# Performance work log

Measured on AMD Instinct MI355X. Metric: run time of the kernel, lower is better.

## Reference

```python
import jax, jax.numpy as jnp
import numpy as np

ALPHA = jnp.full((8,), 0.25, dtype=jnp.float32)  # per-class focal alpha
GAMMA = 2.0
TEMP = 0.07
CIRC_TARGET = 1.0
CIRC_WEIGHT = 0.1
MIN_AGREE = 0.6
W_FOCAL, W_CONTRAST, W_CONSENSUS = 1.0, 0.5, 0.3


def setup_inputs() -> dict:
    key = jax.random.key(0)
    k1, k2, k3, k4, k5 = jax.random.split(key, 5)
    return {
        "logits": jax.random.normal(k1, (32, 8, 256, 256), dtype=jnp.float32),
        "target": jax.random.randint(k2, (32, 256, 256), 0, 8, dtype=jnp.int32),
        "features": jax.random.normal(k3, (1024, 512), dtype=jnp.float32),
        "masks": jax.random.uniform(k4, (32, 3, 256, 256), dtype=jnp.float32),
        "method_preds": jax.random.uniform(k5, (3, 32, 256, 256), dtype=jnp.float32),
    }


def focal_loss(logits, target):
    B, C, H, W = logits.shape
    x = logits.transpose(0, 2, 3, 1).reshape(-1, C)  # [BHW, C]
    t = target.reshape(-1)
    logp = jax.nn.log_softmax(x, axis=-1)
    ce = -jnp.take_along_axis(logp, t[:, None], axis=1)[:, 0]
    p = jnp.exp(-ce)
    focal_w = ALPHA[t] * (1.0 - p) ** GAMMA
    return jnp.mean(focal_w * ce)


def contrastive_loss(features):
    Bf = features.shape[0]
    f = features / jnp.linalg.norm(features, axis=1, keepdims=True)
    sim = (f @ f.T) / TEMP  # [Bf, Bf]
    # default labels = arange(Bf//2) tiled twice -> each sample has exactly one
    # positive: its paired view at index (i + Bf//2) % Bf
    pos_idx = (jnp.arange(Bf) + Bf // 2) % Bf
    pos = sim[jnp.arange(Bf), pos_idx]
    diag = jnp.eye(Bf, dtype=bool)
    # logits row i = {positive_i} U negatives_i = all j != i (single positive case)
    masked = jnp.where(diag, -1e30, sim)
    lse = jax.nn.logsumexp(masked, axis=1)
    return jnp.mean(lse - pos)  # CE with target = the (only) positive


def circularity_loss(masks):
    m = masks[:, 0]  # [B, H, W] core channel
    B = m.shape[0]
    area = jnp.sum(m, axis=(1, 2))
    ex = jnp.sum(jnp.abs(m[:, 1:, :] - m[:, :-1, :]), axis=(1, 2))
    ey = jnp.sum(jnp.abs(m[:, :, 1:] - m[:, :, :-1]), axis=(1, 2))
    per = ex + ey
    circ = 4.0 * np.pi * area / jnp.maximum(per, 1e-12) ** 2
    li = jnp.where((area > 0) & (per > 0), (circ - CIRC_TARGET) ** 2, 0.0)
    return CIRC_WEIGHT * jnp.sum(li) / B


def consensus_loss(method_preds):
    K = method_preds.shape[0]
    total, n = 0.0, 0
    for i in range(K):  # K=3 methods -> 3 pairs (fixed, small)
        for j in range(i + 1, K):
            pi, pj = method_preds[i], method_preds[j]
            inter = jnp.sum(pi * pj)
            union = jnp.sum(pi + pj - pi * pj)
            iou = inter / (union + 1e-6)
            total = total + jax.nn.relu(MIN_AGREE - iou)
            n += 1
    return total / n


def reference(logits, target, features, masks, method_preds):
    return (W_FOCAL * focal_loss(logits, target)
            + W_CONTRAST * contrastive_loss(features)
            + circularity_loss(masks)
            + W_CONSENSUS * consensus_loss(method_preds))
```

## Files before the change

kernel.cpp:

```cpp
#include <hip/hip_runtime.h>
#include <math.h>

#define WS_FOCALP 0
#define WS_CONSP  2048
#define WS_AREAP  14336
#define WS_EXP_   14848
#define WS_EYP_   15360
#define WS_POS    15872
#define WS_PART   16896
#define WS_HI_B   393216
#define WS_LO_B   1441792

typedef __attribute__((ext_vector_type(8))) short bf16x8;
typedef __attribute__((ext_vector_type(4))) float f32x4;

__device__ inline float wave_reduce(float v) {
#pragma unroll
  for (int m = 32; m >= 1; m >>= 1) v += __shfl_xor(v, m);
  return v;
}

__device__ inline unsigned short bf16_rne(float x) {
  union { float f; unsigned u; } v; v.f = x;
  unsigned r = v.u + 0x7FFF + ((v.u >> 16) & 1);
  return (unsigned short)(r >> 16);
}
__device__ inline float bf16_f(unsigned short h) {
  union { unsigned u; float f; } v; v.u = ((unsigned)h) << 16; return v.f;
}

__device__ inline float focal_px(float v0, float v1, float v2, float v3,
                                 float v4, float v5, float v6, float v7, int tt) {
  float mx = fmaxf(fmaxf(fmaxf(v0, v1), fmaxf(v2, v3)),
                   fmaxf(fmaxf(v4, v5), fmaxf(v6, v7)));
  float se = __expf(v0 - mx) + __expf(v1 - mx) + __expf(v2 - mx) + __expf(v3 - mx) +
             __expf(v4 - mx) + __expf(v5 - mx) + __expf(v6 - mx) + __expf(v7 - mx);
  float xt = v0;
  xt = (tt == 1) ? v1 : xt;
  xt = (tt == 2) ? v2 : xt;
  xt = (tt == 3) ? v3 : xt;
  xt = (tt == 4) ? v4 : xt;
  xt = (tt == 5) ? v5 : xt;
  xt = (tt == 6) ? v6 : xt;
  xt = (tt == 7) ? v7 : xt;
  float lp = (xt - mx) - __logf(se);
  float p = __expf(lp);
  float om = 1.0f - p;
  return 0.25f * om * om * (-lp);
}

__global__ __launch_bounds__(256) void prep_kernel(const float* __restrict__ feat,
                                                   float* __restrict__ ws) {
  const int tid = threadIdx.x;
  const int lane = tid & 63;
  const int wid = tid >> 6;
  int row = blockIdx.x * 4 + wid;
  const float4* f4 = (const float4*)feat;
  float4 u = f4[row * 128 + lane];
  float4 w = f4[row * 128 + 64 + lane];
  float s = u.x * u.x + u.y * u.y + u.z * u.z + u.w * u.w +
            w.x * w.x + w.y * w.y + w.z * w.z + w.w * w.w;
  s = wave_reduce(s);
  float scale = 3.7796447300922719f / sqrtf(s);
  float g[8] = {u.x * scale, u.y * scale, u.z * scale, u.w * scale,
                w.x * scale, w.y * scale, w.z * scale, w.w * scale};
  unsigned short h[8];
  unsigned short l[8];
#pragma unroll
  for (int i = 0; i < 8; i++) {
    h[i] = bf16_rne(g[i]);
    l[i] = bf16_rne(g[i] - bf16_f(h[i]));
  }
  char* hb = (char*)ws + WS_HI_B + row * 1024;
  char* lb = (char*)ws + WS_LO_B + row * 1024;
  *(ushort4*)(hb + lane * 8) = make_ushort4(h[0], h[1], h[2], h[3]);
  *(ushort4*)(hb + 512 + lane * 8) = make_ushort4(h[4], h[5], h[6], h[7]);
  *(ushort4*)(lb + lane * 8) = make_ushort4(l[0], l[1], l[2], l[3]);
  *(ushort4*)(lb + 512 + lane * 8) = make_ushort4(l[4], l[5], l[6], l[7]);
}

__global__ __launch_bounds__(256) void fused_kernel(
    const float* __restrict__ logits, const int* __restrict__ target,
    const float* __restrict__ masks, const float* __restrict__ preds,
    float* __restrict__ ws) {
  __shared__ float red[32];
  const int bid = blockIdx.x;
  const int tid = threadIdx.x;
  const int lane = tid & 63;
  const int wid = tid >> 6;

  if (bid < 128) {
    const int rt = bid >> 3, ct = bid & 7;
    const int wr = wid >> 1, wc = wid & 1;
    const int l15 = lane & 15;
    const int hi8 = lane >> 4;
    const char* HI = (const char*)ws + WS_HI_B;
    const char* LO = (const char*)ws + WS_LO_B;
    const int ar = rt * 64 + wr * 32 + l15;
    const int bc = ct * 128 + wc * 64 + l15;
    const int kb16 = hi8 * 16;

    f32x4 acc[2][4];
#pragma unroll
    for (int r = 0; r < 2; r++)
#pragma unroll
      for (int c = 0; c < 4; c++) acc[r][c] = (f32x4){0.f, 0.f, 0.f, 0.f};

#pragma unroll 2
    for (int kb = 0; kb < 16; kb++) {
      int ko = kb * 64 + kb16;
      bf16x8 ah[2], al[2], bh[4], bl[4];
#pragma unroll
      for (int r = 0; r < 2; r++) {
        ah[r] = *(const bf16x8*)(HI + (ar + r * 16) * 1024 + ko);
        al[r] = *(const bf16x8*)(LO + (ar + r * 16) * 1024 + ko);
      }
#pragma unroll
      for (int c = 0; c < 4; c++) {
        bh[c] = *(const bf16x8*)(HI + (bc + c * 16) * 1024 + ko);
        bl[c] = *(const bf16x8*)(LO + (bc + c * 16) * 1024 + ko);
      }
#pragma unroll
      for (int r = 0; r < 2; r++)
#pragma unroll
        for (int c = 0; c < 4; c++) {
          acc[r][c] = __builtin_amdgcn_mfma_f32_16x16x32_bf16(ah[r], bh[c], acc[r][c], 0, 0, 0);
          acc[r][c] = __builtin_amdgcn_mfma_f32_16x16x32_bf16(ah[r], bl[c], acc[r][c], 0, 0, 0);
          acc[r][c] = __builtin_amdgcn_mfma_f32_16x16x32_bf16(al[r], bh[c], acc[r][c], 0, 0, 0);
        }
    }

    float2* part = (float2*)(ws + WS_PART);
#pragma unroll
    for (int r = 0; r < 2; r++)
#pragma unroll
      for (int q = 0; q < 4; q++) {
        int row = rt * 64 + wr * 32 + r * 16 + hi8 * 4 + q;
        int pc = (row + 512) & 1023;
        float m = -3e38f;
        float v[4];
#pragma unroll
        for (int c = 0; c < 4; c++) {
          int col = ct * 128 + wc * 64 + c * 16 + l15;
          float x = acc[r][c][q];
          if (col == pc) ws[WS_POS + row] = x;
          if (col == row) x = -1e30f;
          v[c] = x;
          m = fmaxf(m, x);
        }
        float s = 0.f;
#pragma unroll
        for (int c = 0; c < 4; c++) s += __expf(v[c] - m);
#pragma unroll
        for (int d = 1; d < 16; d <<= 1) {
          float mo = __shfl_xor(m, d), so = __shfl_xor(s, d);
          float nm = fmaxf(m, mo);
          s = s * __expf(m - nm) + so * __expf(mo - nm);
          m = nm;
        }
        if (l15 == 0) part[row * 16 + ct * 2 + wc] = make_float2(m, s);
      }
    return;
  }

  const int bid2 = bid - 128;

  if (bid2 < 2048) {
    int t = bid2 * 256 + tid;
    int p4 = t * 4;
    int b = p4 >> 16;
    int hw = p4 & 65535;
    const float* lb = logits + (b << 19) + hw;
    float4 x0 = *(const float4*)(lb + (0 << 16));
    float4 x1 = *(const float4*)(lb + (1 << 16));
    float4 x2 = *(const float4*)(lb + (2 << 16));
    float4 x3 = *(const float4*)(lb + (3 << 16));
    float4 x4 = *(const float4*)(lb + (4 << 16));
    float4 x5 = *(const float4*)(lb + (5 << 16));
    float4 x6 = *(const float4*)(lb + (6 << 16));
    float4 x7 = *(const float4*)(lb + (7 << 16));
    int4 tg = *(const int4*)(target + p4);
    float acc = 0.0f;
    acc += focal_px(x0.x, x1.x, x2.x, x3.x, x4.x, x5.x, x6.x, x7.x, tg.x);
    acc += focal_px(x0.y, x1.y, x2.y, x3.y, x4.y, x5.y, x6.y, x7.y, tg.y);
    acc += focal_px(x0.z, x1.z, x2.z, x3.z, x4.z, x5.z, x6.z, x7.z, tg.z);
    acc += focal_px(x0.w, x1.w, x2.w, x3.w, x4.w, x5.w, x6.w, x7.w, tg.w);
    float v = wave_reduce(acc);
    if (lane == 0) red[wid] = v;
    __syncthreads();
    if (tid == 0) ws[WS_FOCALP + bid2] = red[0] + red[1] + red[2] + red[3];

  } else if (bid2 < 2560) {
    int bi = bid2 - 2048;
    int img = bi >> 4;
    int part = bi & 15;
    const float* mS = masks + img * 3 * 65536;
    const float4* m4 = (const float4*)mS;
    float a = 0.0f, ex = 0.0f, ey = 0.0f;
#pragma unroll
    for (int i = 0; i < 4; i++) {
      int v = tid + 256 * i;
      int rl = v >> 6;
      int c4 = v & 63;
      int row = part * 16 + rl;
      float4 val = m4[row * 64 + c4];
      a += val.x + val.y + val.z + val.w;
      ey += fabsf(val.y - val.x) + fabsf(val.z - val.y) + fabsf(val.w - val.z);
      if (c4 > 0) ey += fabsf(val.x - mS[row * 256 + c4 * 4 - 1]);
      if (row > 0) {
        float4 u = m4[(row - 1) * 64 + c4];
        ex += fabsf(val.x - u.x) + fabsf(val.y - u.y) +
              fabsf(val.z - u.z) + fabsf(val.w - u.w);
      }
    }
    float ra = wave_reduce(a);
    float rx = wave_reduce(ex);
    float ry = wave_reduce(ey);
    if (lane == 0) {
      red[wid + 0] = ra; red[wid + 4] = rx; red[wid + 8] = ry;
    }
    __syncthreads();
    if (tid == 0) {
      ws[WS_AREAP + bi] = red[0] + red[1] + red[2] + red[3];
      ws[WS_EXP_ + bi] = red[4] + red[5] + red[6] + red[7];
      ws[WS_EYP_ + bi] = red[8] + red[9] + red[10] + red[11];
    }

  } else {
    int b = bid2 - 2560;
    int t = b * 256 + tid;
    const float4* q = (const float4*)preds;
    float4 a0 = q[t];
    float4 a1 = q[t + 524288];
    float4 a2 = q[t + 1048576];
    float s0 = a0.x + a0.y + a0.z + a0.w;
    float s1 = a1.x + a1.y + a1.z + a1.w;
    float s2 = a2.x + a2.y + a2.z + a2.w;
    float p01 = a0.x * a1.x + a0.y * a1.y + a0.z * a1.z + a0.w * a1.w;
    float p02 = a0.x * a2.x + a0.y * a2.y + a0.z * a2.z + a0.w * a2.w;
    float p12 = a1.x * a2.x + a1.y * a2.y + a1.z * a2.z + a1.w * a2.w;
    float r0 = wave_reduce(s0);
    float r1 = wave_reduce(s1);
    float r2 = wave_reduce(s2);
    float r3 = wave_reduce(p01);
    float r4 = wave_reduce(p02);
    float r5 = wave_reduce(p12);
    if (lane == 0) {
      red[wid + 0] = r0; red[wid + 4] = r1; red[wid + 8] = r2;
      red[wid + 12] = r3; red[wid + 16] = r4; red[wid + 20] = r5;
    }
    __syncthreads();
    if (tid == 0) {
#pragma unroll
      for (int k = 0; k < 6; k++)
        ws[WS_CONSP + k * 2048 + b] =
            red[k * 4] + red[k * 4 + 1] + red[k * 4 + 2] + red[k * 4 + 3];
    }
  }
}

__device__ inline float block_reduce_1024(float v, float* red) {
  int tid = threadIdx.x;
  v = wave_reduce(v);
  __syncthreads();
  if ((tid & 63) == 0) red[tid >> 6] = v;
  __syncthreads();
  float t = 0.0f;
  if (tid == 0) {
#pragma unroll
    for (int i = 0; i < 16; i++) t += red[i];
  }
  return t;
}

__global__ __launch_bounds__(1024) void final_kernel(float* __restrict__ ws,
                                                     float* __restrict__ out) {
  __shared__ float red[16];
  __shared__ float li_s[32];
  int r = threadIdx.x;

  const float2* part = (const float2*)(ws + WS_PART);
  float M = -1e30f, S = 0.0f;
#pragma unroll
  for (int ctl = 0; ctl < 16; ctl++) {
    float2 p = part[r * 16 + ctl];
    float nm = fmaxf(M, p.x);
    S = S * __expf(M - nm) + p.y * __expf(p.x - nm);
    M = nm;
  }
  float lse = M + __logf(S);
  float contr_sum = block_reduce_1024(lse - ws[WS_POS + r], red);

  float focal_sum =
      block_reduce_1024(ws[WS_FOCALP + r] + ws[WS_FOCALP + r + 1024], red);

  float cons[6];
#pragma unroll
  for (int k = 0; k < 6; k++) {
    const float* p = ws + WS_CONSP + k * 2048;
    cons[k] = block_reduce_1024(p[r] + p[r + 1024], red);
  }

  float li = 0.0f;
  if (r < 512) {
    float a = ws[WS_AREAP + r];
    float ex = ws[WS_EXP_ + r];
    float ey = ws[WS_EYP_ + r];
#pragma unroll
    for (int d = 1; d < 16; d <<= 1) {
      a += __shfl_xor(a, d);
      ex += __shfl_xor(ex, d);
      ey += __shfl_xor(ey, d);
    }
    if ((r & 15) == 0) {
      float per = ex + ey;
      float dd = fmaxf(per, 1e-12f);
      float c = 12.566370614359172f * a / (dd * dd);
      li = (a > 0.0f && per > 0.0f) ? (c - 1.0f) * (c - 1.0f) : 0.0f;
      li_s[r >> 4] = li;
    }
  }
  __syncthreads();

  if (r == 0) {
    float circ = 0.0f;
#pragma unroll
    for (int i = 0; i < 32; i++) circ += li_s[i];
    circ = 0.1f * circ / 32.0f;

    float contr = contr_sum / 1024.0f;
    float focal = focal_sum / 2097152.0f;

    float S0 = cons[0], S1 = cons[1], S2 = cons[2];
    float P01 = cons[3], P02 = cons[4], P12 = cons[5];
    float co = 0.0f;
    co += fmaxf(0.6f - P01 / (S0 + S1 - P01 + 1e-6f), 0.0f);
    co += fmaxf(0.6f - P02 / (S0 + S2 - P02 + 1e-6f), 0.0f);
    co += fmaxf(0.6f - P12 / (S1 + S2 - P12 + 1e-6f), 0.0f);
    co *= (1.0f / 3.0f);

    out[0] = focal + 0.5f * contr + circ + 0.3f * co;
  }
}

extern "C" void kernel_launch(void* const* d_in, const int* in_sizes, int n_in,
                              void* d_out, int out_size, void* d_ws, size_t ws_size,
                              hipStream_t stream) {
  const float* logits = (const float*)d_in[0];
  const int* target = (const int*)d_in[1];
  const float* feat = (const float*)d_in[2];
  const float* masks = (const float*)d_in[3];
  const float* preds = (const float*)d_in[4];
  float* ws = (float*)d_ws;
  float* out = (float*)d_out;

  prep_kernel<<<256, 256, 0, stream>>>(feat, ws);
  fused_kernel<<<4736, 256, 0, stream>>>(logits, target, masks, preds, ws);
  final_kernel<<<1, 1024, 0, stream>>>(ws, out);
}
```

Measured before the change: 54.36 us.

## Move feature prep into streaming kernel and split similarity GEMM into own kernel

Feature normalisation and bf16 hi/lo splitting now run as extra blocks at the end of the main streaming kernel, which removes the separate prep launch. The similarity GEMM moves to its own kernel afterwards, using smaller 64x64 tiles over 256 blocks so more CUs share the work, which doubles the partial logsumexp entries per row. The final kernel replaces eight sequential block reductions with one batched wave-reduce pass and a single barrier. In exchange, the GEMM no longer overlaps with the bandwidth-bound streaming work and now runs serially after it.

```diff
diff --git a/kernel.cpp b/kernel.cpp
--- a/kernel.cpp
+++ b/kernel.cpp
@@ -49,124 +49,18 @@
   return 0.25f * om * om * (-lp);
 }
 
-__global__ __launch_bounds__(256) void prep_kernel(const float* __restrict__ feat,
-                                                   float* __restrict__ ws) {
-  const int tid = threadIdx.x;
-  const int lane = tid & 63;
-  const int wid = tid >> 6;
-  int row = blockIdx.x * 4 + wid;
-  const float4* f4 = (const float4*)feat;
-  float4 u = f4[row * 128 + lane];
-  float4 w = f4[row * 128 + 64 + lane];
-  float s = u.x * u.x + u.y * u.y + u.z * u.z + u.w * u.w +
-            w.x * w.x + w.y * w.y + w.z * w.z + w.w * w.w;
-  s = wave_reduce(s);
-  float scale = 3.7796447300922719f / sqrtf(s);
-  float g[8] = {u.x * scale, u.y * scale, u.z * scale, u.w * scale,
-                w.x * scale, w.y * scale, w.z * scale, w.w * scale};
-  unsigned short h[8];
-  unsigned short l[8];
-#pragma unroll
-  for (int i = 0; i < 8; i++) {
-    h[i] = bf16_rne(g[i]);
-    l[i] = bf16_rne(g[i] - bf16_f(h[i]));
-  }
-  char* hb = (char*)ws + WS_HI_B + row * 1024;
-  char* lb = (char*)ws + WS_LO_B + row * 1024;
-  *(ushort4*)(hb + lane * 8) = make_ushort4(h[0], h[1], h[2], h[3]);
-  *(ushort4*)(hb + 512 + lane * 8) = make_ushort4(h[4], h[5], h[6], h[7]);
-  *(ushort4*)(lb + lane * 8) = make_ushort4(l[0], l[1], l[2], l[3]);
-  *(ushort4*)(lb + 512 + lane * 8) = make_ushort4(l[4], l[5], l[6], l[7]);
-}
-
-__global__ __launch_bounds__(256) void fused_kernel(
+__global__ __launch_bounds__(256) void mega_kernel(
     const float* __restrict__ logits, const int* __restrict__ target,
-    const float* __restrict__ masks, const float* __restrict__ preds,
-    float* __restrict__ ws) {
+    const float* __restrict__ feat, const float* __restrict__ masks,
+    const float* __restrict__ preds, float* __restrict__ ws) {
   __shared__ float red[32];
   const int bid = blockIdx.x;
   const int tid = threadIdx.x;
   const int lane = tid & 63;
   const int wid = tid >> 6;
 
-  if (bid < 128) {
-    const int rt = bid >> 3, ct = bid & 7;
-    const int wr = wid >> 1, wc = wid & 1;
-    const int l15 = lane & 15;
-    const int hi8 = lane >> 4;
-    const char* HI = (const char*)ws + WS_HI_B;
-    const char* LO = (const char*)ws + WS_LO_B;
-    const int ar = rt * 64 + wr * 32 + l15;
-    const int bc = ct * 128 + wc * 64 + l15;
-    const int kb16 = hi8 * 16;
-
-    f32x4 acc[2][4];
-#pragma unroll
-    for (int r = 0; r < 2; r++)
-#pragma unroll
-      for (int c = 0; c < 4; c++) acc[r][c] = (f32x4){0.f, 0.f, 0.f, 0.f};
-
-#pragma unroll 2
-    for (int kb = 0; kb < 16; kb++) {
-      int ko = kb * 64 + kb16;
-      bf16x8 ah[2], al[2], bh[4], bl[4];
-#pragma unroll
-      for (int r = 0; r < 2; r++) {
-        ah[r] = *(const bf16x8*)(HI + (ar + r * 16) * 1024 + ko);
-        al[r] = *(const bf16x8*)(LO + (ar + r * 16) * 1024 + ko);
-      }
-#pragma unroll
-      for (int c = 0; c < 4; c++) {
-        bh[c] = *(const bf16x8*)(HI + (bc + c * 16) * 1024 + ko);
-        bl[c] = *(const bf16x8*)(LO + (bc + c * 16) * 1024 + ko);
-      }
-#pragma unroll
-      for (int r = 0; r < 2; r++)
-#pragma unroll
-        for (int c = 0; c < 4; c++) {
-          acc[r][c] = __builtin_amdgcn_mfma_f32_16x16x32_bf16(ah[r], bh[c], acc[r][c], 0, 0, 0);
-          acc[r][c] = __builtin_amdgcn_mfma_f32_16x16x32_bf16(ah[r], bl[c], acc[r][c], 0, 0, 0);
-          acc[r][c] = __builtin_amdgcn_mfma_f32_16x16x32_bf16(al[r], bh[c], acc[r][c], 0, 0, 0);
-        }
-    }
-
-    float2* part = (float2*)(ws + WS_PART);
-#pragma unroll
-    for (int r = 0; r < 2; r++)
-#pragma unroll
-      for (int q = 0; q < 4; q++) {
-        int row = rt * 64 + wr * 32 + r * 16 + hi8 * 4 + q;
-        int pc = (row + 512) & 1023;
-        float m = -3e38f;
-        float v[4];
-#pragma unroll
-        for (int c = 0; c < 4; c++) {
-          int col = ct * 128 + wc * 64 + c * 16 + l15;
-          float x = acc[r][c][q];
-          if (col == pc) ws[WS_POS + row] = x;
-          if (col == row) x = -1e30f;
-          v[c] = x;
-          m = fmaxf(m, x);
-        }
-        float s = 0.f;
-#pragma unroll
-        for (int c = 0; c < 4; c++) s += __expf(v[c] - m);
-#pragma unroll
-        for (int d = 1; d < 16; d <<= 1) {
-          float mo = __shfl_xor(m, d), so = __shfl_xor(s, d);
-          float nm = fmaxf(m, mo);
-          s = s * __expf(m - nm) + so * __expf(mo - nm);
-          m = nm;
-        }
-        if (l15 == 0) part[row * 16 + ct * 2 + wc] = make_float2(m, s);
-      }
-    return;
-  }
-
-  const int bid2 = bid - 128;
-
-  if (bid2 < 2048) {
-    int t = bid2 * 256 + tid;
+  if (bid < 2048) {
+    int t = bid * 256 + tid;
     int p4 = t * 4;
     int b = p4 >> 16;
     int hw = p4 & 65535;
@@ -188,10 +82,10 @@
     float v = wave_reduce(acc);
     if (lane == 0) red[wid] = v;
     __syncthreads();
-    if (tid == 0) ws[WS_FOCALP + bid2] = red[0] + red[1] + red[2] + red[3];
-
-  } else if (bid2 < 2560) {
-    int bi = bid2 - 2048;
+    if (tid == 0) ws[WS_FOCALP + bid] = red[0] + red[1] + red[2] + red[3];
+
+  } else if (bid < 2560) {
+    int bi = bid - 2048;
     int img = bi >> 4;
     int part = bi & 15;
     const float* mS = masks + img * 3 * 65536;
@@ -226,8 +120,8 @@
       ws[WS_EYP_ + bi] = red[8] + red[9] + red[10] + red[11];
     }
 
-  } else {
-    int b = bid2 - 2560;
+  } else if (bid < 4608) {
+    int b = bid - 2560;
     int t = b * 256 + tid;
     const float4* q = (const float4*)preds;
     float4 a0 = q[t];
@@ -256,52 +150,138 @@
         ws[WS_CONSP + k * 2048 + b] =
             red[k * 4] + red[k * 4 + 1] + red[k * 4 + 2] + red[k * 4 + 3];
     }
-  }
-}
-
-__device__ inline float block_reduce_1024(float v, float* red) {
-  int tid = threadIdx.x;
-  v = wave_reduce(v);
-  __syncthreads();
-  if ((tid & 63) == 0) red[tid >> 6] = v;
-  __syncthreads();
-  float t = 0.0f;
-  if (tid == 0) {
-#pragma unroll
-    for (int i = 0; i < 16; i++) t += red[i];
-  }
-  return t;
+
+  } else {
+    int row = (bid - 4608) * 4 + wid;
+    const float4* f4 = (const float4*)feat;
+    float4 u = f4[row * 128 + lane];
+    float4 w = f4[row * 128 + 64 + lane];
+    float s = u.x * u.x + u.y * u.y + u.z * u.z + u.w * u.w +
+              w.x * w.x + w.y * w.y + w.z * w.z + w.w * w.w;
+    s = wave_reduce(s);
+    float scale = 3.7796447300922719f / sqrtf(s);
+    float g[8] = {u.x * scale, u.y * scale, u.z * scale, u.w * scale,
+                  w.x * scale, w.y * scale, w.z * scale, w.w * scale};
+    unsigned short h[8];
+    unsigned short l[8];
+#pragma unroll
+    for (int i = 0; i < 8; i++) {
+      h[i] = bf16_rne(g[i]);
+      l[i] = bf16_rne(g[i] - bf16_f(h[i]));
+    }
+    char* hb = (char*)ws + WS_HI_B + row * 1024;
+    char* lb = (char*)ws + WS_LO_B + row * 1024;
+    *(ushort4*)(hb + lane * 8) = make_ushort4(h[0], h[1], h[2], h[3]);
+    *(ushort4*)(hb + 512 + lane * 8) = make_ushort4(h[4], h[5], h[6], h[7]);
+    *(ushort4*)(lb + lane * 8) = make_ushort4(l[0], l[1], l[2], l[3]);
+    *(ushort4*)(lb + 512 + lane * 8) = make_ushort4(l[4], l[5], l[6], l[7]);
+  }
+}
+
+__global__ __launch_bounds__(256) void sim_kernel(float* __restrict__ ws) {
+  const int tid = threadIdx.x;
+  const int lane = tid & 63;
+  const int wid = tid >> 6;
+  const int rt = blockIdx.x >> 4, ct = blockIdx.x & 15;
+  const int wr = wid >> 1, wc = wid & 1;
+  const int l15 = lane & 15;
+  const int hi8 = lane >> 4;
+  const char* HI = (const char*)ws + WS_HI_B;
+  const char* LO = (const char*)ws + WS_LO_B;
+  const int ar = rt * 64 + wr * 32 + l15;
+  const int bc = ct * 64 + wc * 32 + l15;
+  const int kb16 = hi8 * 16;
+
+  f32x4 acc[2][2];
+#pragma unroll
+  for (int r = 0; r < 2; r++)
+#pragma unroll
+    for (int c = 0; c < 2; c++) acc[r][c] = (f32x4){0.f, 0.f, 0.f, 0.f};
+
+#pragma unroll 4
+  for (int kb = 0; kb < 16; kb++) {
+    int ko = kb * 64 + kb16;
+    bf16x8 ah[2], al[2], bh[2], bl[2];
+#pragma unroll
+    for (int r = 0; r < 2; r++) {
+      ah[r] = *(const bf16x8*)(HI + (ar + r * 16) * 1024 + ko);
+      al[r] = *(const bf16x8*)(LO + (ar + r * 16) * 1024 + ko);
+    }
+#pragma unroll
+    for (int c = 0; c < 2; c++) {
+      bh[c] = *(const bf16x8*)(HI + (bc + c * 16) * 1024 + ko);
+      bl[c] = *(const bf16x8*)(LO + (bc + c * 16) * 1024 + ko);
+    }
+#pragma unroll
+    for (int r = 0; r < 2; r++)
+#pragma unroll
+      for (int c = 0; c < 2; c++) {
+        acc[r][c] = __builtin_amdgcn_mfma_f32_16x16x32_bf16(ah[r], bh[c], acc[r][c], 0, 0, 0);
+        acc[r][c] = __builtin_amdgcn_mfma_f32_16x16x32_bf16(ah[r], bl[c], acc[r][c], 0, 0, 0);
+        acc[r][c] = __builtin_amdgcn_mfma_f32_16x16x32_bf16(al[r], bh[c], acc[r][c], 0, 0, 0);
+      }
+  }
+
+  float2* part = (float2*)(ws + WS_PART);
+#pragma unroll
+  for (int r = 0; r < 2; r++)
+#pragma unroll
+    for (int q = 0; q < 4; q++) {
+      int row = rt * 64 + wr * 32 + r * 16 + hi8 * 4 + q;
+      int pc = (row + 512) & 1023;
+      float m = -3e38f;
+      float v[2];
+#pragma unroll
+      for (int c = 0; c < 2; c++) {
+        int col = ct * 64 + wc * 32 + c * 16 + l15;
+        float x = acc[r][c][q];
+        if (col == pc) ws[WS_POS + row] = x;
+        if (col == row) x = -1e30f;
+        v[c] = x;
+        m = fmaxf(m, x);
+      }
+      float s = __expf(v[0] - m) + __expf(v[1] - m);
+#pragma unroll
+      for (int d = 1; d < 16; d <<= 1) {
+        float mo = __shfl_xor(m, d), so = __shfl_xor(s, d);
+        float nm = fmaxf(m, mo);
+        s = s * __expf(m - nm) + so * __expf(mo - nm);
+        m = nm;
+      }
+      if (l15 == 0) part[row * 32 + ct * 2 + wc] = make_float2(m, s);
+    }
 }
 
 __global__ __launch_bounds__(1024) void final_kernel(float* __restrict__ ws,
                                                      float* __restrict__ out) {
-  __shared__ float red[16];
+  __shared__ float red[16][8];
   __shared__ float li_s[32];
   int r = threadIdx.x;
-
+  int lane = r & 63, wid = r >> 6;
+
+  float v[8];
   const float2* part = (const float2*)(ws + WS_PART);
   float M = -1e30f, S = 0.0f;
 #pragma unroll
-  for (int ctl = 0; ctl < 16; ctl++) {
-    float2 p = part[r * 16 + ctl];
+  for (int ctl = 0; ctl < 32; ctl++) {
+    float2 p = part[r * 32 + ctl];
     float nm = fmaxf(M, p.x);
     S = S * __expf(M - nm) + p.y * __expf(p.x - nm);
     M = nm;
   }
-  float lse = M + __logf(S);
-  float contr_sum = block_reduce_1024(lse - ws[WS_POS + r], red);
-
-  float focal_sum =
-      block_reduce_1024(ws[WS_FOCALP + r] + ws[WS_FOCALP + r + 1024], red);
-
-  float cons[6];
+  v[0] = (M + __logf(S)) - ws[WS_POS + r];
+  v[1] = ws[WS_FOCALP + r] + ws[WS_FOCALP + r + 1024];
 #pragma unroll
   for (int k = 0; k < 6; k++) {
     const float* p = ws + WS_CONSP + k * 2048;
-    cons[k] = block_reduce_1024(p[r] + p[r + 1024], red);
-  }
-
-  float li = 0.0f;
+    v[2 + k] = p[r] + p[r + 1024];
+  }
+#pragma unroll
+  for (int k = 0; k < 8; k++) {
+    v[k] = wave_reduce(v[k]);
+    if (lane == 0) red[wid][k] = v[k];
+  }
+
   if (r < 512) {
     float a = ws[WS_AREAP + r];
     float ex = ws[WS_EXP_ + r];
@@ -316,23 +296,30 @@
       float per = ex + ey;
       float dd = fmaxf(per, 1e-12f);
       float c = 12.566370614359172f * a / (dd * dd);
-      li = (a > 0.0f && per > 0.0f) ? (c - 1.0f) * (c - 1.0f) : 0.0f;
-      li_s[r >> 4] = li;
+      li_s[r >> 4] = (a > 0.0f && per > 0.0f) ? (c - 1.0f) * (c - 1.0f) : 0.0f;
     }
   }
   __syncthreads();
 
   if (r == 0) {
+    float tot[8];
+#pragma unroll
+    for (int k = 0; k < 8; k++) {
+      float t = 0.0f;
+#pragma unroll
+      for (int i = 0; i < 16; i++) t += red[i][k];
+      tot[k] = t;
+    }
     float circ = 0.0f;
 #pragma unroll
     for (int i = 0; i < 32; i++) circ += li_s[i];
     circ = 0.1f * circ / 32.0f;
 
-    float contr = contr_sum / 1024.0f;
-    float focal = focal_sum / 2097152.0f;
-
-    float S0 = cons[0], S1 = cons[1], S2 = cons[2];
-    float P01 = cons[3], P02 = cons[4], P12 = cons[5];
+    float contr = tot[0] / 1024.0f;
+    float focal = tot[1] / 2097152.0f;
+
+    float S0 = tot[2], S1 = tot[3], S2 = tot[4];
+    float P01 = tot[5], P02 = tot[6], P12 = tot[7];
     float co = 0.0f;
     co += fmaxf(0.6f - P01 / (S0 + S1 - P01 + 1e-6f), 0.0f);
     co += fmaxf(0.6f - P02 / (S0 + S2 - P02 + 1e-6f), 0.0f);
@@ -354,7 +341,7 @@
   float* ws = (float*)d_ws;
   float* out = (float*)d_out;
 
-  prep_kernel<<<256, 256, 0, stream>>>(feat, ws);
-  fused_kernel<<<4736, 256, 0, stream>>>(logits, target, masks, preds, ws);
+  mega_kernel<<<4864, 256, 0, stream>>>(logits, target, feat, masks, preds, ws);
+  sim_kernel<<<256, 256, 0, stream>>>(ws);
   final_kernel<<<1, 1024, 0, stream>>>(ws, out);
 }
```

Result: slower. 57.13 us (+5.1%).
